# Optimization experiments

Measured on AMD Instinct MI355X. Metric: run time of the kernel, lower is better.

The kernel has to match this reference:

```python
import jax, jax.numpy as jnp
import numpy as np
from jax import lax

SEQ, FEAT, U1, U2, U3, OUT = 20, 5, 10, 7, 4, 4
BATCH = 262144


def _he_uniform(key, shape, fan_in):
    lim = np.sqrt(6.0 / fan_in)
    return jax.random.uniform(key, shape, jnp.float32, -lim, lim)


def _orthogonal(key, n, m):
    a = jax.random.normal(key, (max(n, m), min(n, m)), jnp.float32)
    q, _ = jnp.linalg.qr(a)
    return q[:n, :m] if n >= m else q[:m, :n].T


def _lstm_params(key, in_dim, units):
    k1, k2 = jax.random.split(key)
    Wk = _he_uniform(k1, (in_dim, 4 * units), in_dim)
    Wr = _orthogonal(k2, units, 4 * units)
    # Keras unit_forget_bias: bias = [zeros(i), ones(f), zeros(c), zeros(o)]
    b = jnp.concatenate([jnp.zeros(units), jnp.ones(units), jnp.zeros(2 * units)]).astype(jnp.float32)
    return Wk, Wr, b


def setup_inputs() -> dict:
    key = jax.random.key(0)
    ks = jax.random.split(key, 5)
    x = jax.random.normal(ks[0], (BATCH, SEQ, FEAT), jnp.float32)
    Wk1, Wr1, b1 = _lstm_params(ks[1], FEAT, U1)
    Wk2, Wr2, b2 = _lstm_params(ks[2], U1, U2)
    Wk3, Wr3, b3 = _lstm_params(ks[3], U2, U3)
    kd1, kd2 = jax.random.split(ks[4])
    lim = np.sqrt(6.0 / (U3 + OUT))  # glorot_uniform (Dense default)
    Wd = jax.random.uniform(kd1, (U3, OUT), jnp.float32, -lim, lim)
    bd = jnp.zeros((OUT,), jnp.float32)
    return {"x": x, "Wk1": Wk1, "Wr1": Wr1, "b1": b1,
            "Wk2": Wk2, "Wr2": Wr2, "b2": b2,
            "Wk3": Wk3, "Wr3": Wr3, "b3": b3,
            "Wd": Wd, "bd": bd}


def lstm_layer(x, Wk, Wr, b):
    # x: [B, T, F] -> h-sequence [B, T, U]; Keras gate order i, f, c(g), o
    B = x.shape[0]
    U = Wr.shape[0]
    # precompute input projection for all timesteps (one big GEMM)
    zx = jnp.einsum('btf,fg->btg', x, Wk) + b  # [B, T, 4U]
    zxT = jnp.swapaxes(zx, 0, 1)               # [T, B, 4U]

    def step(carry, zt):
        h, c = carry
        z = zt + h @ Wr
        i, f, g, o = jnp.split(z, 4, axis=-1)
        i = jax.nn.sigmoid(i)
        f = jax.nn.sigmoid(f)
        g = jnp.tanh(g)
        o = jax.nn.sigmoid(o)
        c = f * c + i * g
        h = o * jnp.tanh(c)
        return (h, c), h

    init = (jnp.zeros((B, U), x.dtype), jnp.zeros((B, U), x.dtype))
    _, hs = lax.scan(step, init, zxT)
    return jnp.swapaxes(hs, 0, 1)  # [B, T, U]


def reference(x, Wk1, Wr1, b1, Wk2, Wr2, b2, Wk3, Wr3, b3, Wd, bd):
    h = lstm_layer(x, Wk1, Wr1, b1)
    h = lstm_layer(h, Wk2, Wr2, b2)
    h = lstm_layer(h, Wk3, Wr3, b3)
    return jax.nn.sigmoid(jnp.einsum('btu,uo->bto', h, Wd) + bd)
```

## Files before the change

kernel.cpp:

```cpp
#include <hip/hip_runtime.h>

static constexpr int SEQ = 20, FEAT = 5, NU1 = 10, NU2 = 7, NU3 = 4, NOUT = 4;

typedef short bf16x8 __attribute__((ext_vector_type(8)));
typedef float f32x4  __attribute__((ext_vector_type(4)));
typedef float f32x2  __attribute__((ext_vector_type(2)));

static constexpr unsigned ONE_P = 0x3F803F80u;


__device__ __forceinline__ unsigned short bf16_hi_rne(float x) {
    unsigned u = __float_as_uint(x);
    return (unsigned short)((u + 0x7FFF + ((u >> 16) & 1)) >> 16);
}
__device__ __forceinline__ unsigned short bf16_trunc(float x) {
    return (unsigned short)(__float_as_uint(x) >> 16);
}
__device__ __forceinline__ float bf16_to_f(unsigned short h) {
    return __uint_as_float(((unsigned)h) << 16);
}
__device__ __forceinline__ unsigned hpack(float h) {
    unsigned rp;
    asm("v_cvt_pk_bf16_f32 %0, %1, %1" : "=v"(rp) : "v"(h));
    float lo = h - __uint_as_float(rp << 16);
    return __builtin_amdgcn_perm(__float_as_uint(lo), rp, 0x07060100u);
}

__device__ __forceinline__ float sigm(float x) {
    return __builtin_amdgcn_rcpf(1.0f + __builtin_amdgcn_exp2f(x * -1.4426950408889634f));
}
__device__ __forceinline__ float ftanh(float x) {
    return 1.0f - 2.0f * __builtin_amdgcn_rcpf(1.0f + __builtin_amdgcn_exp2f(x * 2.8853900817779268f));
}

__device__ __forceinline__ unsigned act_unit(const f32x4 z, float& c) {
    f32x2 a = {z[0], z[1]};
    a = a * (-1.4426950408889634f);
    f32x2 ea = {__builtin_amdgcn_exp2f(a[0]), __builtin_amdgcn_exp2f(a[1])};
    ea = ea + 1.0f;
    const float gi = __builtin_amdgcn_rcpf(ea[0]);
    const float gf = __builtin_amdgcn_rcpf(ea[1]);
    const f32x2 sc = {2.8853900817779268f, -1.4426950408889634f};
    f32x2 b = {z[2], z[3]};
    b = b * sc;
    f32x2 eb = {__builtin_amdgcn_exp2f(b[0]), __builtin_amdgcn_exp2f(b[1])};
    eb = eb + 1.0f;
    const float rg = __builtin_amdgcn_rcpf(eb[0]);
    const float go = __builtin_amdgcn_rcpf(eb[1]);
    const float gg = 1.0f - 2.0f * rg;
    c = gf * c + gi * gg;
    return hpack(go * ftanh(c));
}

__device__ __forceinline__ unsigned bperm(int idx, unsigned v) {
    return (unsigned)__builtin_amdgcn_ds_bpermute(idx, (int)v);
}
__device__ __forceinline__ bf16x8 bfrag(unsigned v0, unsigned v1) {
    uint4 u{v0, v0, v1, v1};
    return __builtin_bit_cast(bf16x8, u);
}
__device__ __forceinline__ f32x4 MF(bf16x8 a, bf16x8 b, f32x4 c) {
    return __builtin_amdgcn_mfma_f32_16x16x32_bf16(a, b, c, 0, 0, 0);
}

__global__ void build_afrags(const float* Wk1, const float* Wr1, const float* b1,
                             const float* Wk2, const float* Wr2, const float* b2,
                             const float* Wk3, const float* Wr3, const float* b3,
                             const float* Wd,  const float* bd, unsigned* ws) {
    const int lane = threadIdx.x;
    const int m = lane & 15;
    const int qh = lane >> 4;

    for (int tau = 0; tau < 3; ++tau)
    for (int kap = 0; kap < 2; ++kap) {
        unsigned short h8[8];
        for (int j = 0; j < 8; ++j) {
            const int k = kap * 32 + qh * 8 + j;
            const int i = k >> 2, cls = k & 3;
            const int u = tau * 4 + (m >> 2), col = (m & 3) * NU1 + u;
            unsigned short v = 0;
            if (u < NU1) {
                if (i < 15) {
                    float W;
                    if (i < 8)       W = Wr1[((i >> 1) + 4 * (i & 1)) * 40 + col];
                    else if (i < 10) W = Wr1[i * 40 + col];
                    else             W = Wk1[(i - 10) * 40 + col];
                    unsigned short hi = bf16_hi_rne(W);
                    v = (cls < 2) ? hi : bf16_trunc(W - bf16_to_f(hi));
                } else if (i == 15) {
                    float bv = b1[col];
                    unsigned short hi = bf16_hi_rne(bv);
                    v = (cls == 0) ? hi : ((cls == 1) ? bf16_trunc(bv - bf16_to_f(hi)) : (unsigned short)0);
                }
            }
            h8[j] = v;
        }
        const int id = tau * 2 + kap;
        for (int d = 0; d < 4; ++d)
            ws[id * 256 + lane * 4 + d] = (unsigned)h8[2 * d] | ((unsigned)h8[2 * d + 1] << 16);
    }
    for (int tau = 0; tau < 2; ++tau)
    for (int kap = 0; kap < 3; ++kap) {
        unsigned short h8[8];
        for (int j = 0; j < 8; ++j) {
            const int k = kap * 32 + qh * 8 + j;
            const int i = k >> 2, cls = k & 3;
            const int u = tau * 4 + (m >> 2), col = (m & 3) * NU2 + u;
            unsigned short v = 0;
            if (u < NU2) {
                if (i < 17) {
                    float W;
                    if (i < 8)        W = Wk2[((i >> 1) + 4 * (i & 1)) * 28 + col];
                    else if (i < 10)  W = Wk2[i * 28 + col];
                    else if (i < 16)  W = Wr2[(((i - 10) >> 1) + 4 * ((i - 10) & 1)) * 28 + col];
                    else              W = Wr2[3 * 28 + col];
                    unsigned short hi = bf16_hi_rne(W);
                    v = (cls < 2) ? hi : bf16_trunc(W - bf16_to_f(hi));
                } else if (i == 17) {
                    float bv = b2[col];
                    unsigned short hi = bf16_hi_rne(bv);
                    v = (cls == 0) ? hi : ((cls == 1) ? bf16_trunc(bv - bf16_to_f(hi)) : (unsigned short)0);
                }
            }
            h8[j] = v;
        }
        const int id = 6 + tau * 3 + kap;
        for (int d = 0; d < 4; ++d)
            ws[id * 256 + lane * 4 + d] = (unsigned)h8[2 * d] | ((unsigned)h8[2 * d + 1] << 16);
    }
    for (int kap = 0; kap < 2; ++kap) {
        unsigned short h8[8];
        for (int j = 0; j < 8; ++j) {
            const int k = kap * 32 + qh * 8 + j;
            const int i = k >> 2, cls = k & 3;
            const int u = m >> 2, col = (m & 3) * NU3 + u;
            unsigned short v = 0;
            if (i < 11) {
                float W;
                if (i < 6)       W = Wk3[((i >> 1) + 4 * (i & 1)) * 16 + col];
                else if (i == 6) W = Wk3[3 * 16 + col];
                else             W = Wr3[(i - 7) * 16 + col];
                unsigned short hi = bf16_hi_rne(W);
                v = (cls < 2) ? hi : bf16_trunc(W - bf16_to_f(hi));
            } else if (i == 11) {
                float bv = b3[col];
                unsigned short hi = bf16_hi_rne(bv);
                v = (cls == 0) ? hi : ((cls == 1) ? bf16_trunc(bv - bf16_to_f(hi)) : (unsigned short)0);
            }
            h8[j] = v;
        }
        const int id = 12 + kap;
        for (int d = 0; d < 4; ++d)
            ws[id * 256 + lane * 4 + d] = (unsigned)h8[2 * d] | ((unsigned)h8[2 * d + 1] << 16);
    }
    {
        unsigned short h8[8];
        for (int j = 0; j < 8; ++j) {
            const int k = qh * 8 + j;
            const int i = k >> 2, cls = k & 3;
            unsigned short v = 0;
            if (i < 4) {
                float W = Wd[i * NOUT + (m & 3)];
                unsigned short hi = bf16_hi_rne(W);
                v = (cls < 2) ? hi : bf16_trunc(W - bf16_to_f(hi));
            } else if (i == 4) {
                float bv = bd[m & 3];
                unsigned short hi = bf16_hi_rne(bv);
                v = (cls == 0) ? hi : ((cls == 1) ? bf16_trunc(bv - bf16_to_f(hi)) : (unsigned short)0);
            }
            h8[j] = v;
        }
        for (int d = 0; d < 4; ++d)
            ws[14 * 256 + lane * 4 + d] = (unsigned)h8[2 * d] | ((unsigned)h8[2 * d + 1] << 16);
    }
}

__global__ __launch_bounds__(256, 4) void lstm3_mfma(
    const float* __restrict__ x, const unsigned* __restrict__ wsA,
    float* __restrict__ out, int B) {
    const int tid = threadIdx.x;
    const int lane = tid & 63;
    const int n = lane & 15;
    const int q = lane >> 4;

    bf16x8 af[15];
#pragma unroll
    for (int i = 0; i < 15; ++i) {
        uint4 v = ((const uint4*)wsA)[i * 64 + lane];
        af[i] = __builtin_bit_cast(bf16x8, v);
    }

    const int i_h19 = (n + 16) << 2;
    const int i_sh  = (n + 16 * ((q + 3) & 3)) << 2;
    const int i_r1  = (n + 16 * ((q + 1) & 3)) << 2;
    const int i_r2  = (n + 16 * ((q + 2) & 3)) << 2;

    const f32x4 zro = {0.f, 0.f, 0.f, 0.f};

    const int ngrp = B >> 4;
    const int gw = (blockIdx.x * blockDim.x + tid) >> 6;
    const int nw = (gridDim.x * blockDim.x) >> 6;

    for (int grp = gw; grp < ngrp; grp += nw) {
        const float* xr = x + (size_t)grp * 16 * (SEQ * FEAT) + n * (SEQ * FEAT);
        float* ob = out + (size_t)grp * 16 * (SEQ * NOUT) + n * (SEQ * NOUT);

        unsigned p1a = 0, p1b = 0, p1c = 0, t9 = 0;
        unsigned p2a = 0, p2b = 0, p3 = 0, rot = 0, rot2 = 0;
        float c10 = 0.f, c11 = 0.f, c12 = 0.f, c20 = 0.f, c21 = 0.f, c30 = 0.f;
        float d0 = 0.f, d1 = 0.f, d2 = 0.f, d3 = 0.f;

        float xa = 0.f, xc = 0.f;
        if (q != 0) {
            const float* p = xr + 2 * (q - 1);
            xa = p[0];
            if (q != 3) xc = p[1];
        }

#pragma unroll 1
        for (int t = 0; t < SEQ; ++t) {
            const unsigned xP0 = hpack(xa), xP1 = hpack(xc);
            {
                const int tn = (t + 1 < SEQ) ? t + 1 : 0;
                if (q != 0) {
                    const float* p = xr + tn * FEAT + 2 * (q - 1);
                    xa = p[0];
                    if (q != 3) xc = p[1];
                }
            }
            bf16x8 bF0 = bfrag(p1a, p1b);
            unsigned F1v0 = (q == 0) ? p1c : xP0;
            unsigned F1v1 = (q == 0) ? t9 : ((q == 3) ? ONE_P : xP1);
            bf16x8 bF1 = bfrag(F1v0, F1v1);
            f32x4 z0 = MF(af[0], bF0, zro); z0 = MF(af[1], bF1, z0);
            f32x4 z1 = MF(af[2], bF0, zro); z1 = MF(af[3], bF1, z1);
            f32x4 z2 = MF(af[4], bF0, zro); z2 = MF(af[5], bF1, z2);
            const unsigned s2a = bperm(i_sh, p2a);
            const unsigned s2b = bperm(i_sh, p2b);
            p1a = act_unit(z0, c10);
            p1b = act_unit(z1, c11);
            p1c = act_unit(z2, c12);
            t9  = bperm(i_h19, p1c);
            bf16x8 bA  = bfrag(p1a, p1b);
            unsigned F2v0 = (q == 0) ? p1c : s2a;
            unsigned F2v1 = (q == 0) ? t9  : s2b;
            bf16x8 bF2 = bfrag(F2v0, F2v1);
            bf16x8 bF3 = bfrag(s2a, ONE_P);
            f32x4 y0 = MF(af[6], bA, zro);
            y0 = MF(af[7], bF2, y0);
            y0 = MF(af[8], bF3, y0);
            f32x4 y1 = MF(af[9], bA, zro);
            y1 = MF(af[10], bF2, y1);
            y1 = MF(af[11], bF3, y1);
            p2a = act_unit(y0, c20);
            p2b = act_unit(y1, c21);
            bf16x8 bF4 = bfrag(p2a, (q == 3) ? rot : p2b);
            unsigned F5v0 = (q == 0) ? rot  : rot2;
            unsigned F5v1 = (q == 0) ? rot2 : ONE_P;
            bf16x8 bF5 = bfrag(F5v0, F5v1);
            f32x4 w0 = MF(af[12], bF4, zro);
            w0 = MF(af[13], bF5, w0);
            p3 = act_unit(w0, c30);
            rot  = bperm(i_r1, p3);
            rot2 = bperm(i_r2, p3);
            unsigned F6v0 = (q == 0) ? p3 : ((q == 1) ? rot : ONE_P);
            unsigned F6v1 = (q == 0) ? rot : rot2;
            f32x4 o0 = MF(af[14], bfrag(F6v0, F6v1), zro);
            {
                float v01 = (q & 1) ? o0[1] : o0[0];
                float v23 = (q & 1) ? o0[3] : o0[2];
                float v = (q & 2) ? v23 : v01;
                const int r = t & 3;
                d0 = (r == 0) ? v : d0;
                d1 = (r == 1) ? v : d1;
                d2 = (r == 2) ? v : d2;
                d3 = (r == 3) ? v : d3;
            }
            if ((t & 3) == 3) {
                float* p = ob + (t - 3) * NOUT + q;
                p[0 * NOUT] = sigm(d0);
                p[1 * NOUT] = sigm(d1);
                p[2 * NOUT] = sigm(d2);
                p[3 * NOUT] = sigm(d3);
            }
        }
    }
}

extern "C" void kernel_launch(void* const* d_in, const int* in_sizes, int n_in,
                              void* d_out, int out_size, void* d_ws, size_t ws_size,
                              hipStream_t stream) {
    const float* x   = (const float*)d_in[0];
    const float* Wk1 = (const float*)d_in[1];
    const float* Wr1 = (const float*)d_in[2];
    const float* b1  = (const float*)d_in[3];
    const float* Wk2 = (const float*)d_in[4];
    const float* Wr2 = (const float*)d_in[5];
    const float* b2  = (const float*)d_in[6];
    const float* Wk3 = (const float*)d_in[7];
    const float* Wr3 = (const float*)d_in[8];
    const float* b3  = (const float*)d_in[9];
    const float* Wd  = (const float*)d_in[10];
    const float* bd  = (const float*)d_in[11];
    float* out = (float*)d_out;
    unsigned* ws = (unsigned*)d_ws;

    const int B = in_sizes[0] / (SEQ * FEAT);

    build_afrags<<<1, 64, 0, stream>>>(Wk1, Wr1, b1, Wk2, Wr2, b2,
                                       Wk3, Wr3, b3, Wd, bd, ws);
    lstm3_mfma<<<4096, 256, 0, stream>>>(x, ws, out, B);
}
```

Baseline: 378.6 us.

## Compress MFMA A-fragments to half registers and fuse LSTM gate reciprocals

Stores the split-bf16 weight fragments in a compact 2-dword form per lane and expands them to the 8-element MFMA operand with v_perm just before each MFMA. An empty asm barrier stops the compiler from hoisting the expansion back out. This halves the persistent register footprint for weights, and launch bounds are raised from 4 to 5 blocks per SM to use the freed registers for occupancy. The activation unit is also rewritten algebraically to merge the sigmoid/tanh reciprocals into two rcp calls, which adds extra perm instructions per MFMA and some risk to numerical range or precision.

```diff
diff --git a/kernel.cpp b/kernel.cpp
--- a/kernel.cpp
+++ b/kernel.cpp
@@ -4,9 +4,8 @@
 
 typedef short bf16x8 __attribute__((ext_vector_type(8)));
 typedef float f32x4  __attribute__((ext_vector_type(4)));
-typedef float f32x2  __attribute__((ext_vector_type(2)));
-
-static constexpr unsigned ONE_P = 0x3F803F80u;
+
+static constexpr unsigned ONE_P = 0x00003F80u;
 
 
 __device__ __forceinline__ unsigned short bf16_hi_rne(float x) {
@@ -29,27 +28,22 @@
 __device__ __forceinline__ float sigm(float x) {
     return __builtin_amdgcn_rcpf(1.0f + __builtin_amdgcn_exp2f(x * -1.4426950408889634f));
 }
-__device__ __forceinline__ float ftanh(float x) {
-    return 1.0f - 2.0f * __builtin_amdgcn_rcpf(1.0f + __builtin_amdgcn_exp2f(x * 2.8853900817779268f));
-}
 
 __device__ __forceinline__ unsigned act_unit(const f32x4 z, float& c) {
-    f32x2 a = {z[0], z[1]};
-    a = a * (-1.4426950408889634f);
-    f32x2 ea = {__builtin_amdgcn_exp2f(a[0]), __builtin_amdgcn_exp2f(a[1])};
-    ea = ea + 1.0f;
-    const float gi = __builtin_amdgcn_rcpf(ea[0]);
-    const float gf = __builtin_amdgcn_rcpf(ea[1]);
-    const f32x2 sc = {2.8853900817779268f, -1.4426950408889634f};
-    f32x2 b = {z[2], z[3]};
-    b = b * sc;
-    f32x2 eb = {__builtin_amdgcn_exp2f(b[0]), __builtin_amdgcn_exp2f(b[1])};
-    eb = eb + 1.0f;
-    const float rg = __builtin_amdgcn_rcpf(eb[0]);
-    const float go = __builtin_amdgcn_rcpf(eb[1]);
-    const float gg = 1.0f - 2.0f * rg;
-    c = gf * c + gi * gg;
-    return hpack(go * ftanh(c));
+    const float L2E = 1.4426950408889634f;
+    float ei = __builtin_amdgcn_exp2f(z[0] * -L2E);
+    float ef = __builtin_amdgcn_exp2f(z[1] * -L2E);
+    float eg = __builtin_amdgcn_exp2f(z[2] * (2.0f * L2E));
+    float eo = __builtin_amdgcn_exp2f(z[3] * -L2E);
+    float di = 1.0f + ei, df = 1.0f + ef, dg = 1.0f + eg;
+    float m1 = di * dg;
+    float num = c * m1 + (eg - 1.0f) * df;
+    float r = __builtin_amdgcn_rcpf(df * m1);
+    c = num * r;
+    float ec = __builtin_amdgcn_exp2f(c * (2.0f * L2E));
+    float r2 = __builtin_amdgcn_rcpf((1.0f + eo) * (1.0f + ec));
+    float h = (ec - 1.0f) * r2;
+    return hpack(h);
 }
 
 __device__ __forceinline__ unsigned bperm(int idx, unsigned v) {
@@ -59,8 +53,15 @@
     uint4 u{v0, v0, v1, v1};
     return __builtin_bit_cast(bf16x8, u);
 }
-__device__ __forceinline__ f32x4 MF(bf16x8 a, bf16x8 b, f32x4 c) {
-    return __builtin_amdgcn_mfma_f32_16x16x32_bf16(a, b, c, 0, 0, 0);
+__device__ __forceinline__ f32x4 MFc(uint2 cf, bf16x8 b, f32x4 acc) {
+    asm volatile("" : "+v"(cf.x), "+v"(cf.y));
+    unsigned d0 = __builtin_amdgcn_perm(cf.x, cf.x, 0x01000100u);
+    unsigned d1 = __builtin_amdgcn_perm(cf.x, cf.x, 0x03020302u);
+    unsigned d2 = __builtin_amdgcn_perm(cf.y, cf.y, 0x01000100u);
+    unsigned d3 = __builtin_amdgcn_perm(cf.y, cf.y, 0x03020302u);
+    uint4 u{d0, d1, d2, d3};
+    return __builtin_amdgcn_mfma_f32_16x16x32_bf16(
+        __builtin_bit_cast(bf16x8, u), b, acc, 0, 0, 0);
 }
 
 __global__ void build_afrags(const float* Wk1, const float* Wr1, const float* b1,
@@ -73,109 +74,88 @@
 
     for (int tau = 0; tau < 3; ++tau)
     for (int kap = 0; kap < 2; ++kap) {
-        unsigned short h8[8];
-        for (int j = 0; j < 8; ++j) {
-            const int k = kap * 32 + qh * 8 + j;
-            const int i = k >> 2, cls = k & 3;
+        unsigned short h4[2][2];
+        for (int ii = 0; ii < 2; ++ii) {
+            const int i = kap * 8 + qh * 2 + ii;
             const int u = tau * 4 + (m >> 2), col = (m & 3) * NU1 + u;
-            unsigned short v = 0;
-            if (u < NU1) {
-                if (i < 15) {
-                    float W;
-                    if (i < 8)       W = Wr1[((i >> 1) + 4 * (i & 1)) * 40 + col];
-                    else if (i < 10) W = Wr1[i * 40 + col];
-                    else             W = Wk1[(i - 10) * 40 + col];
-                    unsigned short hi = bf16_hi_rne(W);
-                    v = (cls < 2) ? hi : bf16_trunc(W - bf16_to_f(hi));
-                } else if (i == 15) {
-                    float bv = b1[col];
-                    unsigned short hi = bf16_hi_rne(bv);
-                    v = (cls == 0) ? hi : ((cls == 1) ? bf16_trunc(bv - bf16_to_f(hi)) : (unsigned short)0);
-                }
-            }
-            h8[j] = v;
+            unsigned short hi = 0, lo = 0;
+            if (u < NU1 && i <= 15) {
+                float W;
+                if (i < 8)       W = Wr1[((i >> 1) + 4 * (i & 1)) * 40 + col];
+                else if (i < 10) W = Wr1[i * 40 + col];
+                else if (i < 15) W = Wk1[(i - 10) * 40 + col];
+                else             W = b1[col];
+                hi = bf16_hi_rne(W);
+                lo = bf16_trunc(W - bf16_to_f(hi));
+            }
+            h4[ii][0] = hi; h4[ii][1] = lo;
         }
         const int id = tau * 2 + kap;
-        for (int d = 0; d < 4; ++d)
-            ws[id * 256 + lane * 4 + d] = (unsigned)h8[2 * d] | ((unsigned)h8[2 * d + 1] << 16);
+        ws[id * 128 + lane * 2 + 0] = (unsigned)h4[0][0] | ((unsigned)h4[0][1] << 16);
+        ws[id * 128 + lane * 2 + 1] = (unsigned)h4[1][0] | ((unsigned)h4[1][1] << 16);
     }
     for (int tau = 0; tau < 2; ++tau)
     for (int kap = 0; kap < 3; ++kap) {
-        unsigned short h8[8];
-        for (int j = 0; j < 8; ++j) {
-            const int k = kap * 32 + qh * 8 + j;
-            const int i = k >> 2, cls = k & 3;
+        unsigned short h4[2][2];
+        for (int ii = 0; ii < 2; ++ii) {
+            const int i = kap * 8 + qh * 2 + ii;
             const int u = tau * 4 + (m >> 2), col = (m & 3) * NU2 + u;
-            unsigned short v = 0;
-            if (u < NU2) {
-                if (i < 17) {
-                    float W;
-                    if (i < 8)        W = Wk2[((i >> 1) + 4 * (i & 1)) * 28 + col];
-                    else if (i < 10)  W = Wk2[i * 28 + col];
-                    else if (i < 16)  W = Wr2[(((i - 10) >> 1) + 4 * ((i - 10) & 1)) * 28 + col];
-                    else              W = Wr2[3 * 28 + col];
-                    unsigned short hi = bf16_hi_rne(W);
-                    v = (cls < 2) ? hi : bf16_trunc(W - bf16_to_f(hi));
-                } else if (i == 17) {
-                    float bv = b2[col];
-                    unsigned short hi = bf16_hi_rne(bv);
-                    v = (cls == 0) ? hi : ((cls == 1) ? bf16_trunc(bv - bf16_to_f(hi)) : (unsigned short)0);
-                }
-            }
-            h8[j] = v;
+            unsigned short hi = 0, lo = 0;
+            if (u < NU2 && i <= 17) {
+                float W;
+                if (i < 8)        W = Wk2[((i >> 1) + 4 * (i & 1)) * 28 + col];
+                else if (i < 10)  W = Wk2[i * 28 + col];
+                else if (i < 16)  W = Wr2[(((i - 10) >> 1) + 4 * ((i - 10) & 1)) * 28 + col];
+                else if (i == 16) W = Wr2[3 * 28 + col];
+                else              W = b2[col];
+                hi = bf16_hi_rne(W);
+                lo = bf16_trunc(W - bf16_to_f(hi));
+            }
+            h4[ii][0] = hi; h4[ii][1] = lo;
         }
         const int id = 6 + tau * 3 + kap;
-        for (int d = 0; d < 4; ++d)
-            ws[id * 256 + lane * 4 + d] = (unsigned)h8[2 * d] | ((unsigned)h8[2 * d + 1] << 16);
+        ws[id * 128 + lane * 2 + 0] = (unsigned)h4[0][0] | ((unsigned)h4[0][1] << 16);
+        ws[id * 128 + lane * 2 + 1] = (unsigned)h4[1][0] | ((unsigned)h4[1][1] << 16);
     }
     for (int kap = 0; kap < 2; ++kap) {
-        unsigned short h8[8];
-        for (int j = 0; j < 8; ++j) {
-            const int k = kap * 32 + qh * 8 + j;
-            const int i = k >> 2, cls = k & 3;
+        unsigned short h4[2][2];
+        for (int ii = 0; ii < 2; ++ii) {
+            const int i = kap * 8 + qh * 2 + ii;
             const int u = m >> 2, col = (m & 3) * NU3 + u;
-            unsigned short v = 0;
-            if (i < 11) {
+            unsigned short hi = 0, lo = 0;
+            if (i <= 11) {
                 float W;
                 if (i < 6)       W = Wk3[((i >> 1) + 4 * (i & 1)) * 16 + col];
                 else if (i == 6) W = Wk3[3 * 16 + col];
-                else             W = Wr3[(i - 7) * 16 + col];
-                unsigned short hi = bf16_hi_rne(W);
-                v = (cls < 2) ? hi : bf16_trunc(W - bf16_to_f(hi));
-            } else if (i == 11) {
-                float bv = b3[col];
-                unsigned short hi = bf16_hi_rne(bv);
-                v = (cls == 0) ? hi : ((cls == 1) ? bf16_trunc(bv - bf16_to_f(hi)) : (unsigned short)0);
-            }
-            h8[j] = v;
+                else if (i < 11) W = Wr3[(i - 7) * 16 + col];
+                else             W = b3[col];
+                hi = bf16_hi_rne(W);
+                lo = bf16_trunc(W - bf16_to_f(hi));
+            }
+            h4[ii][0] = hi; h4[ii][1] = lo;
         }
         const int id = 12 + kap;
-        for (int d = 0; d < 4; ++d)
-            ws[id * 256 + lane * 4 + d] = (unsigned)h8[2 * d] | ((unsigned)h8[2 * d + 1] << 16);
+        ws[id * 128 + lane * 2 + 0] = (unsigned)h4[0][0] | ((unsigned)h4[0][1] << 16);
+        ws[id * 128 + lane * 2 + 1] = (unsigned)h4[1][0] | ((unsigned)h4[1][1] << 16);
     }
     {
-        unsigned short h8[8];
-        for (int j = 0; j < 8; ++j) {
-            const int k = qh * 8 + j;
-            const int i = k >> 2, cls = k & 3;
-            unsigned short v = 0;
-            if (i < 4) {
-                float W = Wd[i * NOUT + (m & 3)];
-                unsigned short hi = bf16_hi_rne(W);
-                v = (cls < 2) ? hi : bf16_trunc(W - bf16_to_f(hi));
-            } else if (i == 4) {
-                float bv = bd[m & 3];
-                unsigned short hi = bf16_hi_rne(bv);
-                v = (cls == 0) ? hi : ((cls == 1) ? bf16_trunc(bv - bf16_to_f(hi)) : (unsigned short)0);
-            }
-            h8[j] = v;
-        }
-        for (int d = 0; d < 4; ++d)
-            ws[14 * 256 + lane * 4 + d] = (unsigned)h8[2 * d] | ((unsigned)h8[2 * d + 1] << 16);
-    }
-}
-
-__global__ __launch_bounds__(256, 4) void lstm3_mfma(
+        unsigned short h4[2][2];
+        for (int ii = 0; ii < 2; ++ii) {
+            const int i = qh * 2 + ii;
+            unsigned short hi = 0, lo = 0;
+            if (i <= 4) {
+                float W = (i < 4) ? Wd[i * NOUT + (m & 3)] : bd[m & 3];
+                hi = bf16_hi_rne(W);
+                lo = bf16_trunc(W - bf16_to_f(hi));
+            }
+            h4[ii][0] = hi; h4[ii][1] = lo;
+        }
+        ws[14 * 128 + lane * 2 + 0] = (unsigned)h4[0][0] | ((unsigned)h4[0][1] << 16);
+        ws[14 * 128 + lane * 2 + 1] = (unsigned)h4[1][0] | ((unsigned)h4[1][1] << 16);
+    }
+}
+
+__global__ __launch_bounds__(256, 5) void lstm3_mfma(
     const float* __restrict__ x, const unsigned* __restrict__ wsA,
     float* __restrict__ out, int B) {
     const int tid = threadIdx.x;
@@ -183,12 +163,10 @@
     const int n = lane & 15;
     const int q = lane >> 4;
 
-    bf16x8 af[15];
+    uint2 cf[15];
 #pragma unroll
-    for (int i = 0; i < 15; ++i) {
-        uint4 v = ((const uint4*)wsA)[i * 64 + lane];
-        af[i] = __builtin_bit_cast(bf16x8, v);
-    }
+    for (int i = 0; i < 15; ++i)
+        cf[i] = ((const uint2*)wsA)[i * 64 + lane];
 
     const int i_h19 = (n + 16) << 2;
     const int i_sh  = (n + 16 * ((q + 3) & 3)) << 2;
@@ -232,9 +210,9 @@
             unsigned F1v0 = (q == 0) ? p1c : xP0;
             unsigned F1v1 = (q == 0) ? t9 : ((q == 3) ? ONE_P : xP1);
             bf16x8 bF1 = bfrag(F1v0, F1v1);
-            f32x4 z0 = MF(af[0], bF0, zro); z0 = MF(af[1], bF1, z0);
-            f32x4 z1 = MF(af[2], bF0, zro); z1 = MF(af[3], bF1, z1);
-            f32x4 z2 = MF(af[4], bF0, zro); z2 = MF(af[5], bF1, z2);
+            f32x4 z0 = MFc(cf[0], bF0, zro); z0 = MFc(cf[1], bF1, z0);
+            f32x4 z1 = MFc(cf[2], bF0, zro); z1 = MFc(cf[3], bF1, z1);
+            f32x4 z2 = MFc(cf[4], bF0, zro); z2 = MFc(cf[5], bF1, z2);
             const unsigned s2a = bperm(i_sh, p2a);
             const unsigned s2b = bperm(i_sh, p2b);
             p1a = act_unit(z0, c10);
@@ -246,26 +224,26 @@
             unsigned F2v1 = (q == 0) ? t9  : s2b;
             bf16x8 bF2 = bfrag(F2v0, F2v1);
             bf16x8 bF3 = bfrag(s2a, ONE_P);
-            f32x4 y0 = MF(af[6], bA, zro);
-            y0 = MF(af[7], bF2, y0);
-            y0 = MF(af[8], bF3, y0);
-            f32x4 y1 = MF(af[9], bA, zro);
-            y1 = MF(af[10], bF2, y1);
-            y1 = MF(af[11], bF3, y1);
+            f32x4 y0 = MFc(cf[6], bA, zro);
+            y0 = MFc(cf[7], bF2, y0);
+            y0 = MFc(cf[8], bF3, y0);
+            f32x4 y1 = MFc(cf[9], bA, zro);
+            y1 = MFc(cf[10], bF2, y1);
+            y1 = MFc(cf[11], bF3, y1);
             p2a = act_unit(y0, c20);
             p2b = act_unit(y1, c21);
             bf16x8 bF4 = bfrag(p2a, (q == 3) ? rot : p2b);
             unsigned F5v0 = (q == 0) ? rot  : rot2;
             unsigned F5v1 = (q == 0) ? rot2 : ONE_P;
             bf16x8 bF5 = bfrag(F5v0, F5v1);
-            f32x4 w0 = MF(af[12], bF4, zro);
-            w0 = MF(af[13], bF5, w0);
+            f32x4 w0 = MFc(cf[12], bF4, zro);
+            w0 = MFc(cf[13], bF5, w0);
             p3 = act_unit(w0, c30);
             rot  = bperm(i_r1, p3);
             rot2 = bperm(i_r2, p3);
             unsigned F6v0 = (q == 0) ? p3 : ((q == 1) ? rot : ONE_P);
             unsigned F6v1 = (q == 0) ? rot : rot2;
-            f32x4 o0 = MF(af[14], bfrag(F6v0, F6v1), zro);
+            f32x4 o0 = MFc(cf[14], bfrag(F6v0, F6v1), zro);
             {
                 float v01 = (q & 1) ? o0[1] : o0[0];
                 float v23 = (q & 1) ? o0[3] : o0[2];
```

Measured after the change: 380.1 us. No clear change (+0.4%).

## Stage weight fragments in LDS and merge LSTM gate reciprocals

Applied to the files above, without the earlier changes.

Moves the 15 bf16 A-fragment weight registers per lane into shared memory and reloads them from LDS every timestep. An opaque offset stops the compiler from hoisting those loads back into registers, and the launch bound rises to 6 waves per SIMD so more wavefronts can hide latency. The gate activation is rewritten algebraically to fold the sigmoid and tanh reciprocals into two rcp calls per unit instead of five. The cost is extra LDS traffic on the serial recurrence path and possible overflow or precision loss in the products of large exponentials.

```diff
diff --git a/kernel.cpp b/kernel.cpp
--- a/kernel.cpp
+++ b/kernel.cpp
@@ -4,7 +4,6 @@
 
 typedef short bf16x8 __attribute__((ext_vector_type(8)));
 typedef float f32x4  __attribute__((ext_vector_type(4)));
-typedef float f32x2  __attribute__((ext_vector_type(2)));
 
 static constexpr unsigned ONE_P = 0x3F803F80u;
 
@@ -29,27 +28,22 @@
 __device__ __forceinline__ float sigm(float x) {
     return __builtin_amdgcn_rcpf(1.0f + __builtin_amdgcn_exp2f(x * -1.4426950408889634f));
 }
-__device__ __forceinline__ float ftanh(float x) {
-    return 1.0f - 2.0f * __builtin_amdgcn_rcpf(1.0f + __builtin_amdgcn_exp2f(x * 2.8853900817779268f));
-}
 
 __device__ __forceinline__ unsigned act_unit(const f32x4 z, float& c) {
-    f32x2 a = {z[0], z[1]};
-    a = a * (-1.4426950408889634f);
-    f32x2 ea = {__builtin_amdgcn_exp2f(a[0]), __builtin_amdgcn_exp2f(a[1])};
-    ea = ea + 1.0f;
-    const float gi = __builtin_amdgcn_rcpf(ea[0]);
-    const float gf = __builtin_amdgcn_rcpf(ea[1]);
-    const f32x2 sc = {2.8853900817779268f, -1.4426950408889634f};
-    f32x2 b = {z[2], z[3]};
-    b = b * sc;
-    f32x2 eb = {__builtin_amdgcn_exp2f(b[0]), __builtin_amdgcn_exp2f(b[1])};
-    eb = eb + 1.0f;
-    const float rg = __builtin_amdgcn_rcpf(eb[0]);
-    const float go = __builtin_amdgcn_rcpf(eb[1]);
-    const float gg = 1.0f - 2.0f * rg;
-    c = gf * c + gi * gg;
-    return hpack(go * ftanh(c));
+    const float L2E = 1.4426950408889634f;
+    float ei = __builtin_amdgcn_exp2f(z[0] * -L2E);
+    float ef = __builtin_amdgcn_exp2f(z[1] * -L2E);
+    float eg = __builtin_amdgcn_exp2f(z[2] * (2.0f * L2E));
+    float eo = __builtin_amdgcn_exp2f(z[3] * -L2E);
+    float di = 1.0f + ei, df = 1.0f + ef, dg = 1.0f + eg;
+    float m1 = di * dg;
+    float num = c * m1 + (eg - 1.0f) * df;
+    float r = __builtin_amdgcn_rcpf(df * m1);
+    c = num * r;
+    float ec = __builtin_amdgcn_exp2f(c * (2.0f * L2E));
+    float r2 = __builtin_amdgcn_rcpf((1.0f + eo) * (1.0f + ec));
+    float h = (ec - 1.0f) * r2;
+    return hpack(h);
 }
 
 __device__ __forceinline__ unsigned bperm(int idx, unsigned v) {
@@ -175,20 +169,20 @@
     }
 }
 
-__global__ __launch_bounds__(256, 4) void lstm3_mfma(
+__global__ __launch_bounds__(256, 6) void lstm3_mfma(
     const float* __restrict__ x, const unsigned* __restrict__ wsA,
     float* __restrict__ out, int B) {
+    __shared__ __attribute__((aligned(16))) unsigned ldsA[15 * 256];
+
     const int tid = threadIdx.x;
     const int lane = tid & 63;
     const int n = lane & 15;
     const int q = lane >> 4;
 
-    bf16x8 af[15];
 #pragma unroll
-    for (int i = 0; i < 15; ++i) {
-        uint4 v = ((const uint4*)wsA)[i * 64 + lane];
-        af[i] = __builtin_bit_cast(bf16x8, v);
-    }
+    for (int i = 0; i < 15; ++i)
+        ldsA[i * 256 + tid] = wsA[i * 256 + tid];
+    __syncthreads();
 
     const int i_h19 = (n + 16) << 2;
     const int i_sh  = (n + 16 * ((q + 3) & 3)) << 2;
@@ -200,6 +194,8 @@
     const int ngrp = B >> 4;
     const int gw = (blockIdx.x * blockDim.x + tid) >> 6;
     const int nw = (gridDim.x * blockDim.x) >> 6;
+
+    unsigned off = 0;
 
     for (int grp = gw; grp < ngrp; grp += nw) {
         const float* xr = x + (size_t)grp * 16 * (SEQ * FEAT) + n * (SEQ * FEAT);
@@ -219,6 +215,10 @@
 
 #pragma unroll 1
         for (int t = 0; t < SEQ; ++t) {
+            asm volatile("" : "+v"(off));
+            const unsigned* Sf = ldsA + lane * 4 + off;
+#define LDF(id) (*(const bf16x8*)(Sf + (id) * 256))
+
             const unsigned xP0 = hpack(xa), xP1 = hpack(xc);
             {
                 const int tn = (t + 1 < SEQ) ? t + 1 : 0;
@@ -232,9 +232,9 @@
             unsigned F1v0 = (q == 0) ? p1c : xP0;
             unsigned F1v1 = (q == 0) ? t9 : ((q == 3) ? ONE_P : xP1);
             bf16x8 bF1 = bfrag(F1v0, F1v1);
-            f32x4 z0 = MF(af[0], bF0, zro); z0 = MF(af[1], bF1, z0);
-            f32x4 z1 = MF(af[2], bF0, zro); z1 = MF(af[3], bF1, z1);
-            f32x4 z2 = MF(af[4], bF0, zro); z2 = MF(af[5], bF1, z2);
+            f32x4 z0 = MF(LDF(0), bF0, zro); z0 = MF(LDF(1), bF1, z0);
+            f32x4 z1 = MF(LDF(2), bF0, zro); z1 = MF(LDF(3), bF1, z1);
+            f32x4 z2 = MF(LDF(4), bF0, zro); z2 = MF(LDF(5), bF1, z2);
             const unsigned s2a = bperm(i_sh, p2a);
             const unsigned s2b = bperm(i_sh, p2b);
             p1a = act_unit(z0, c10);
@@ -246,26 +246,26 @@
             unsigned F2v1 = (q == 0) ? t9  : s2b;
             bf16x8 bF2 = bfrag(F2v0, F2v1);
             bf16x8 bF3 = bfrag(s2a, ONE_P);
-            f32x4 y0 = MF(af[6], bA, zro);
-            y0 = MF(af[7], bF2, y0);
-            y0 = MF(af[8], bF3, y0);
-            f32x4 y1 = MF(af[9], bA, zro);
-            y1 = MF(af[10], bF2, y1);
-            y1 = MF(af[11], bF3, y1);
+            f32x4 y0 = MF(LDF(6), bA, zro);
+            y0 = MF(LDF(7), bF2, y0);
+            y0 = MF(LDF(8), bF3, y0);
+            f32x4 y1 = MF(LDF(9), bA, zro);
+            y1 = MF(LDF(10), bF2, y1);
+            y1 = MF(LDF(11), bF3, y1);
             p2a = act_unit(y0, c20);
             p2b = act_unit(y1, c21);
             bf16x8 bF4 = bfrag(p2a, (q == 3) ? rot : p2b);
             unsigned F5v0 = (q == 0) ? rot  : rot2;
             unsigned F5v1 = (q == 0) ? rot2 : ONE_P;
             bf16x8 bF5 = bfrag(F5v0, F5v1);
-            f32x4 w0 = MF(af[12], bF4, zro);
-            w0 = MF(af[13], bF5, w0);
+            f32x4 w0 = MF(LDF(12), bF4, zro);
+            w0 = MF(LDF(13), bF5, w0);
             p3 = act_unit(w0, c30);
             rot  = bperm(i_r1, p3);
             rot2 = bperm(i_r2, p3);
             unsigned F6v0 = (q == 0) ? p3 : ((q == 1) ? rot : ONE_P);
             unsigned F6v1 = (q == 0) ? rot : rot2;
-            f32x4 o0 = MF(af[14], bfrag(F6v0, F6v1), zro);
+            f32x4 o0 = MF(LDF(14), bfrag(F6v0, F6v1), zro);
             {
                 float v01 = (q & 1) ? o0[1] : o0[0];
                 float v23 = (q & 1) ? o0[3] : o0[2];
@@ -283,6 +283,7 @@
                 p[2 * NOUT] = sigm(d2);
                 p[3 * NOUT] = sigm(d3);
             }
+#undef LDF
         }
     }
 }
```

Result: faster. 363.8 us (-3.9%).
